# Kernel optimization log

Measured on AMD Instinct MI355X. Metric: run time of the kernel, lower is better.

Reference implementation:

```python
import jax, jax.numpy as jnp
import numpy as np

B = 32768
N_PATCH = 196  # 14x14 grid of 2x2 patches over a 28x28 image
DIM = 16       # 2^4 state-vector dimension for 4 wires


def setup_inputs() -> dict:
    key = jax.random.key(0)
    kx, = jax.random.split(key, 1)
    # pixel data in [0,1] like normalized MNIST
    x = jax.random.uniform(kx, (B, 784), dtype=jnp.float32)
    # fixed random 2-qubit layer composed into a single real orthogonal 16x16 unitary
    rng = np.random.default_rng(0)
    q, _ = np.linalg.qr(rng.standard_normal((DIM, DIM)))
    U = jnp.asarray(q, dtype=jnp.float32)
    return {"x": x, "U": U}


def _pauli_z_signs():
    # Z[w, b] = +1 if bit w of basis index b is 0 else -1 (wire 0 = MSB, kron order)
    wires = jnp.arange(4)[:, None]
    basis = jnp.arange(DIM)[None, :]
    bits = (basis >> (3 - wires)) & 1
    return 1.0 - 2.0 * bits.astype(jnp.float32)  # [4, 16]


def reference(x, U):
    bsz = x.shape[0]
    img = x.reshape(bsz, 28, 28)
    # extract 2x2 patches in the same row-major order as the original loop:
    # data = [x[r,c], x[r,c+1], x[r+1,c], x[r+1,c+1]] -> [B, 196, 4]
    data = img.reshape(bsz, 14, 2, 14, 2).transpose(0, 1, 3, 2, 4).reshape(bsz, N_PATCH, 4)
    # RY(theta)|0> = cos(theta/2)|0> + sin(theta/2)|1> per wire (real amplitudes)
    half = 0.5 * data
    q = jnp.stack([jnp.cos(half), jnp.sin(half)], axis=-1)  # [B, 196, 4, 2]
    # product state via kron over the 4 wires -> [B, 196, 16]
    state = jnp.einsum('bpi,bpj,bpk,bpl->bpijkl',
                       q[:, :, 0], q[:, :, 1], q[:, :, 2], q[:, :, 3]
                       ).reshape(bsz, N_PATCH, DIM)
    # apply the fixed random layer unitary
    state = jnp.einsum('bpd,ed->bpe', state, U)
    # PauliZ expectation on each wire from |amp|^2
    probs = state * state
    Z = _pauli_z_signs()  # [4, 16]
    meas = jnp.einsum('bpd,wd->bpw', probs, Z)  # [B, 196, 4]
    return meas.reshape(bsz, N_PATCH * 4)
```

## Files before the change

kernel.cpp:

```cpp
#include <hip/hip_runtime.h>

typedef _Float16 half4 __attribute__((ext_vector_type(4)));
typedef _Float16 h2 __attribute__((ext_vector_type(2)));
typedef __fp16 fp16x2 __attribute__((ext_vector_type(2)));
typedef float f32x4 __attribute__((ext_vector_type(4)));

#define SINCONST 0.07957747154594767f

__global__ __launch_bounds__(256) void quanv(
    const float* __restrict__ x,
    const float* __restrict__ U,
    float* __restrict__ out,
    int total, int ipw, int rem)
{
    __shared__ __align__(16) unsigned int smem[4 * 2 * 1536 / 4];

    const int tid  = threadIdx.x;
    const int lane = tid & 63;
    const int wib  = tid >> 6;
    const int wave = (blockIdx.x * 256 + tid) >> 6;
    const int p16  = lane & 15;
    const int g    = lane >> 4;

    unsigned int* wsmem = smem + wib * (2 * 1536 / 4);

    half4 aU;
    {
        const float* up = U + p16 * 16 + 4 * g;
        aU[0] = (_Float16)up[0];
        aU[1] = (_Float16)up[1];
        aU[2] = (_Float16)up[2];
        aU[3] = (_Float16)up[3];
    }
    half4 aS;
    {
        int w = p16 & 3;
        #pragma unroll
        for (int i = 0; i < 4; ++i) {
            int e = 4 * g + i;
            aS[i] = ((e >> (3 - w)) & 1) ? (_Float16)-1.f : (_Float16)1.f;
        }
    }

    int cnt = ipw + (wave < rem ? 1 : 0);
    if (cnt <= 0) return;
    const int mac0 = wave * ipw + (wave < rem ? wave : rem);

    int P0 = mac0 * 64 + lane;
    int pc = P0 < total ? P0 : total - 1;
    int img = pc / 196;
    int pp  = pc - img * 196;
    int bo  = img * 784;

    float2 curT, curB, nxtT, nxtB;
    {
        int r = (pp * 2341) >> 15;
        const float2* ptr = reinterpret_cast<const float2*>(x + bo + 2 * pp + 28 * r);
        curT = ptr[0];
        curB = ptr[14];
    }

    for (int j = 0; j < cnt; ++j) {
        const int pbase = (mac0 + j) * 64;

        if (j + 1 < cnt) {
            pp += 64;
            if (pp >= 196) { pp -= 196; bo += 784; }
            int r = (pp * 2341) >> 15;
            const float2* ptr = reinterpret_cast<const float2*>(x + bo + 2 * pp + 28 * r);
            nxtT = ptr[0];
            nxtB = ptr[14];
        }

        float r0 = curT.x * SINCONST, r1 = curT.y * SINCONST;
        float r2 = curB.x * SINCONST, r3 = curB.y * SINCONST;
        float s0 = __builtin_amdgcn_sinf(r0), c0 = __builtin_amdgcn_cosf(r0);
        float s1 = __builtin_amdgcn_sinf(r1), c1 = __builtin_amdgcn_cosf(r1);
        float s2 = __builtin_amdgcn_sinf(r2), c2 = __builtin_amdgcn_cosf(r2);
        float s3 = __builtin_amdgcn_sinf(r3), c3 = __builtin_amdgcn_cosf(r3);

        float a0 = c0 * c1, a1 = c0 * s1, a2 = s0 * c1, a3 = s0 * s1;
        float q0 = c2 * c3, q1 = c2 * s3, q2 = s2 * c3, q3 = s2 * s3;

        uint4 ad;
        ad.x = __builtin_bit_cast(unsigned int, __builtin_amdgcn_cvt_pkrtz(a0, a0));
        ad.y = __builtin_bit_cast(unsigned int, __builtin_amdgcn_cvt_pkrtz(a1, a1));
        ad.z = __builtin_bit_cast(unsigned int, __builtin_amdgcn_cvt_pkrtz(a2, a2));
        ad.w = __builtin_bit_cast(unsigned int, __builtin_amdgcn_cvt_pkrtz(a3, a3));
        uint2 qd;
        qd.x = __builtin_bit_cast(unsigned int, __builtin_amdgcn_cvt_pkrtz(q0, q1));
        qd.y = __builtin_bit_cast(unsigned int, __builtin_amdgcn_cvt_pkrtz(q2, q3));

        unsigned int* buf = wsmem + (j & 1) * (1536 / 4);
        *reinterpret_cast<uint4*>(buf + lane * 4) = ad;
        *reinterpret_cast<uint2*>(buf + 256 + lane * 2) = qd;

        const unsigned int* adArr = buf;
        const uint2* qArr = reinterpret_cast<const uint2*>(buf + 256);

        #pragma unroll
        for (int t = 0; t < 4; ++t) {
            const int pt = t * 16 + p16;
            unsigned int adw = adArr[pt * 4 + g];
            uint2 qw = qArr[pt];

            h2 ag  = __builtin_bit_cast(h2, adw);
            h2 q01 = __builtin_bit_cast(h2, qw.x);
            h2 q23 = __builtin_bit_cast(h2, qw.y);
            h2 blo = ag * q01;
            h2 bhi = ag * q23;
            half4 bST = __builtin_shufflevector(blo, bhi, 0, 1, 2, 3);

            const f32x4 zero4 = {0.f, 0.f, 0.f, 0.f};
            f32x4 y = __builtin_amdgcn_mfma_f32_16x16x16f16(aU, bST, zero4, 0, 0, 0);

            h2 y01 = __builtin_bit_cast(h2, __builtin_amdgcn_cvt_pkrtz(y[0], y[1]));
            h2 y23 = __builtin_bit_cast(h2, __builtin_amdgcn_cvt_pkrtz(y[2], y[3]));
            h2 p01 = y01 * y01;
            h2 p23 = y23 * y23;
            half4 bP = __builtin_shufflevector(p01, p23, 0, 1, 2, 3);

            f32x4 m = __builtin_amdgcn_mfma_f32_16x16x16f16(aS, bP, zero4, 0, 0, 0);

            int Ps = pbase + pt;
            if (g == 0 && Ps < total) {
                float4 res = make_float4(m[0], m[1], m[2], m[3]);
                *reinterpret_cast<float4*>(out + (size_t)Ps * 4) = res;
            }
        }

        if (j + 1 < cnt) { curT = nxtT; curB = nxtB; }
    }
}

extern "C" void kernel_launch(void* const* d_in, const int* in_sizes, int n_in,
                              void* d_out, int out_size, void* d_ws, size_t ws_size,
                              hipStream_t stream) {
    const float* x = (const float*)d_in[0];
    const float* U = (const float*)d_in[1];
    float* out = (float*)d_out;

    int B = in_sizes[0] / 784;
    int total = B * 196;
    int nmac = (total + 63) / 64;

    int nblocks = 2048;
    int nwaves = nblocks * (256 / 64);
    int ipw = nmac / nwaves;
    int rem = nmac % nwaves;

    quanv<<<nblocks, 256, 0, stream>>>(x, U, out, total, ipw, rem);
}
```

Measured before the change: 38.86 us.

## Process two patches per lane with float4 loads and two-deep prefetch

Each lane now handles a horizontally adjacent pair of 2x2 patches, so it loads 16-byte float4 rows instead of float2 and computes two sets of factors per iteration. Each wave iteration covers 128 patches with 8 MFMA tiles instead of 4. The prefetch now runs two iterations ahead to hide more global memory latency. This widens memory transactions and raises work per wave, at the cost of more registers and larger per-wave LDS buffers. It assumes total is even, which holds because 196 is even.

```diff
diff --git a/kernel.cpp b/kernel.cpp
--- a/kernel.cpp
+++ b/kernel.cpp
@@ -2,10 +2,27 @@
 
 typedef _Float16 half4 __attribute__((ext_vector_type(4)));
 typedef _Float16 h2 __attribute__((ext_vector_type(2)));
-typedef __fp16 fp16x2 __attribute__((ext_vector_type(2)));
 typedef float f32x4 __attribute__((ext_vector_type(4)));
 
 #define SINCONST 0.07957747154594767f
+
+__device__ __forceinline__ unsigned int pk(float a, float b) {
+    return __builtin_bit_cast(unsigned int, __builtin_amdgcn_cvt_pkrtz(a, b));
+}
+
+__device__ __forceinline__ void factors(float px0, float px1, float px2, float px3,
+                                        uint4& ad, uint2& qd) {
+    float t0 = px0 * SINCONST, t1 = px1 * SINCONST;
+    float t2 = px2 * SINCONST, t3 = px3 * SINCONST;
+    float s0 = __builtin_amdgcn_sinf(t0), c0 = __builtin_amdgcn_cosf(t0);
+    float s1 = __builtin_amdgcn_sinf(t1), c1 = __builtin_amdgcn_cosf(t1);
+    float s2 = __builtin_amdgcn_sinf(t2), c2 = __builtin_amdgcn_cosf(t2);
+    float s3 = __builtin_amdgcn_sinf(t3), c3 = __builtin_amdgcn_cosf(t3);
+    float a0 = c0 * c1, a1 = c0 * s1, a2 = s0 * c1, a3 = s0 * s1;
+    float q0 = c2 * c3, q1 = c2 * s3, q2 = s2 * c3, q3 = s2 * s3;
+    ad.x = pk(a0, a0); ad.y = pk(a1, a1); ad.z = pk(a2, a2); ad.w = pk(a3, a3);
+    qd.x = pk(q0, q1); qd.y = pk(q2, q3);
+}
 
 __global__ __launch_bounds__(256) void quanv(
     const float* __restrict__ x,
@@ -13,7 +30,7 @@
     float* __restrict__ out,
     int total, int ipw, int rem)
 {
-    __shared__ __align__(16) unsigned int smem[4 * 2 * 1536 / 4];
+    __shared__ __align__(16) unsigned int smem[4 * 2 * 768];
 
     const int tid  = threadIdx.x;
     const int lane = tid & 63;
@@ -22,7 +39,7 @@
     const int p16  = lane & 15;
     const int g    = lane >> 4;
 
-    unsigned int* wsmem = smem + wib * (2 * 1536 / 4);
+    unsigned int* wsmem = smem + wib * (2 * 768);
 
     half4 aU;
     {
@@ -45,64 +62,45 @@
     int cnt = ipw + (wave < rem ? 1 : 0);
     if (cnt <= 0) return;
     const int mac0 = wave * ipw + (wave < rem ? wave : rem);
+    const int nPairs = total >> 1;
 
-    int P0 = mac0 * 64 + lane;
-    int pc = P0 < total ? P0 : total - 1;
-    int img = pc / 196;
-    int pp  = pc - img * 196;
-    int bo  = img * 784;
+    auto ldp = [&](int j, float4& t4, float4& b4) {
+        int PR = (mac0 + j) * 64 + lane;
+        if (PR >= nPairs) PR = nPairs - 1;
+        int P   = PR * 2;
+        int img = P / 196;
+        int pp  = P - img * 196;
+        int r   = (pp * 2341) >> 15;
+        const float4* ptr = reinterpret_cast<const float4*>(x + img * 784 + 2 * pp + 28 * r);
+        t4 = ptr[0];
+        b4 = ptr[7];
+    };
 
-    float2 curT, curB, nxtT, nxtB;
-    {
-        int r = (pp * 2341) >> 15;
-        const float2* ptr = reinterpret_cast<const float2*>(x + bo + 2 * pp + 28 * r);
-        curT = ptr[0];
-        curB = ptr[14];
-    }
+    float4 cT, cB, nT, nB;
+    ldp(0, cT, cB);
+    nT = cT; nB = cB;
+    if (cnt > 1) ldp(1, nT, nB);
 
     for (int j = 0; j < cnt; ++j) {
-        const int pbase = (mac0 + j) * 64;
+        float4 fT = nT, fB = nB;
+        if (j + 2 < cnt) ldp(j + 2, fT, fB);
 
-        if (j + 1 < cnt) {
-            pp += 64;
-            if (pp >= 196) { pp -= 196; bo += 784; }
-            int r = (pp * 2341) >> 15;
-            const float2* ptr = reinterpret_cast<const float2*>(x + bo + 2 * pp + 28 * r);
-            nxtT = ptr[0];
-            nxtB = ptr[14];
-        }
+        uint4 adA, adB; uint2 qdA, qdB;
+        factors(cT.x, cT.y, cB.x, cB.y, adA, qdA);
+        factors(cT.z, cT.w, cB.z, cB.w, adB, qdB);
 
-        float r0 = curT.x * SINCONST, r1 = curT.y * SINCONST;
-        float r2 = curB.x * SINCONST, r3 = curB.y * SINCONST;
-        float s0 = __builtin_amdgcn_sinf(r0), c0 = __builtin_amdgcn_cosf(r0);
-        float s1 = __builtin_amdgcn_sinf(r1), c1 = __builtin_amdgcn_cosf(r1);
-        float s2 = __builtin_amdgcn_sinf(r2), c2 = __builtin_amdgcn_cosf(r2);
-        float s3 = __builtin_amdgcn_sinf(r3), c3 = __builtin_amdgcn_cosf(r3);
+        unsigned int* buf = wsmem + (j & 1) * 768;
+        *reinterpret_cast<uint4*>(buf + 8 * lane)     = adA;
+        *reinterpret_cast<uint4*>(buf + 8 * lane + 4) = adB;
+        uint4 qq = make_uint4(qdA.x, qdA.y, qdB.x, qdB.y);
+        *reinterpret_cast<uint4*>(buf + 512 + 4 * lane) = qq;
 
-        float a0 = c0 * c1, a1 = c0 * s1, a2 = s0 * c1, a3 = s0 * s1;
-        float q0 = c2 * c3, q1 = c2 * s3, q2 = s2 * c3, q3 = s2 * s3;
-
-        uint4 ad;
-        ad.x = __builtin_bit_cast(unsigned int, __builtin_amdgcn_cvt_pkrtz(a0, a0));
-        ad.y = __builtin_bit_cast(unsigned int, __builtin_amdgcn_cvt_pkrtz(a1, a1));
-        ad.z = __builtin_bit_cast(unsigned int, __builtin_amdgcn_cvt_pkrtz(a2, a2));
-        ad.w = __builtin_bit_cast(unsigned int, __builtin_amdgcn_cvt_pkrtz(a3, a3));
-        uint2 qd;
-        qd.x = __builtin_bit_cast(unsigned int, __builtin_amdgcn_cvt_pkrtz(q0, q1));
-        qd.y = __builtin_bit_cast(unsigned int, __builtin_amdgcn_cvt_pkrtz(q2, q3));
-
-        unsigned int* buf = wsmem + (j & 1) * (1536 / 4);
-        *reinterpret_cast<uint4*>(buf + lane * 4) = ad;
-        *reinterpret_cast<uint2*>(buf + 256 + lane * 2) = qd;
-
-        const unsigned int* adArr = buf;
-        const uint2* qArr = reinterpret_cast<const uint2*>(buf + 256);
-
+        const int pbase = (mac0 + j) * 128;
         #pragma unroll
-        for (int t = 0; t < 4; ++t) {
+        for (int t = 0; t < 8; ++t) {
             const int pt = t * 16 + p16;
-            unsigned int adw = adArr[pt * 4 + g];
-            uint2 qw = qArr[pt];
+            unsigned int adw = buf[pt * 4 + g];
+            uint2 qw = *reinterpret_cast<const uint2*>(buf + 512 + 2 * pt);
 
             h2 ag  = __builtin_bit_cast(h2, adw);
             h2 q01 = __builtin_bit_cast(h2, qw.x);
@@ -114,8 +112,8 @@
             const f32x4 zero4 = {0.f, 0.f, 0.f, 0.f};
             f32x4 y = __builtin_amdgcn_mfma_f32_16x16x16f16(aU, bST, zero4, 0, 0, 0);
 
-            h2 y01 = __builtin_bit_cast(h2, __builtin_amdgcn_cvt_pkrtz(y[0], y[1]));
-            h2 y23 = __builtin_bit_cast(h2, __builtin_amdgcn_cvt_pkrtz(y[2], y[3]));
+            h2 y01 = __builtin_bit_cast(h2, pk(y[0], y[1]));
+            h2 y23 = __builtin_bit_cast(h2, pk(y[2], y[3]));
             h2 p01 = y01 * y01;
             h2 p23 = y23 * y23;
             half4 bP = __builtin_shufflevector(p01, p23, 0, 1, 2, 3);
@@ -129,7 +127,8 @@
             }
         }
 
-        if (j + 1 < cnt) { curT = nxtT; curB = nxtB; }
+        cT = nT; cB = nB;
+        nT = fT; nB = fB;
     }
 }
 
@@ -142,7 +141,8 @@
 
     int B = in_sizes[0] / 784;
     int total = B * 196;
-    int nmac = (total + 63) / 64;
+    int nPairs = total / 2;
+    int nmac = (nPairs + 63) / 64;
 
     int nblocks = 2048;
     int nwaves = nblocks * (256 / 64);
```

After: 40.56 us. +4.4%, slower.
